# Kernel optimization log

Hardware: AMD Instinct MI355X
Metric: run time of the kernel (lower is better)

Reference implementation:

```python
import jax, jax.numpy as jnp
import numpy as np
from jax import lax

IN_F = 512   # encoder output dim
MEL = 80     # mel bins (memory_dim)
R = 7        # reduction factor
ATT = 128    # attention dim
B = 64
T_ENC = 512
T_MEL = 700  # must be divisible by R -> 100 decoder steps


def _gru(x, h, w_ih, w_hh, b_ih, b_hh):
    # torch.nn.GRUCell math
    gi = x @ w_ih.T + b_ih
    gh = h @ w_hh.T + b_hh
    ir, iz, inn = jnp.split(gi, 3, axis=-1)
    hr, hz, hn = jnp.split(gh, 3, axis=-1)
    r = jax.nn.sigmoid(ir + hr)
    z = jax.nn.sigmoid(iz + hz)
    return (1.0 - z) * jnp.tanh(inn + r * hn) + z * h


_PARAM_SHAPES = {
    'prenet_w1': (256, MEL), 'prenet_b1': (256,),
    'prenet_w2': (128, 256), 'prenet_b2': (128,),
    'attrnn_w_ih': (768, IN_F + 128), 'attrnn_w_hh': (768, 256),
    'attrnn_b_ih': (768,), 'attrnn_b_hh': (768,),
    'q_w': (ATT, 256), 'inp_w': (ATT, IN_F), 'v_w': (1, ATT), 'v_b': (1,),
    'loc_conv': (32, 2, 31), 'loc_w': (ATT, 32),
    'pd_w': (256, 256 + IN_F), 'pd_b': (256,),
    'dec1_w_ih': (768, 256), 'dec1_w_hh': (768, 256), 'dec1_b_ih': (768,), 'dec1_b_hh': (768,),
    'dec2_w_ih': (768, 256), 'dec2_w_hh': (768, 256), 'dec2_b_ih': (768,), 'dec2_b_hh': (768,),
    'mel_w': (MEL * R, 256), 'mel_b': (MEL * R,),
    'stop_w': (1, 256 + MEL * R), 'stop_b': (1,),
}


def setup_inputs() -> dict:
    key = jax.random.key(0)
    ks = iter(jax.random.split(key, 40))
    d = {
        'inputs': jax.random.normal(next(ks), (B, T_ENC, IN_F), jnp.float32),
        'memory': jax.random.normal(next(ks), (B, T_MEL, MEL), jnp.float32),
        'mask': jnp.ones((B, T_ENC), dtype=bool),
    }
    for n, s in _PARAM_SHAPES.items():
        d[n] = jax.random.normal(next(ks), s, jnp.float32) * 0.02
    return d


def reference(inputs, memory, mask, prenet_w1, prenet_b1, prenet_w2, prenet_b2,
              attrnn_w_ih, attrnn_w_hh, attrnn_b_ih, attrnn_b_hh,
              q_w, inp_w, v_w, v_b, loc_conv, loc_w, pd_w, pd_b,
              dec1_w_ih, dec1_w_hh, dec1_b_ih, dec1_b_hh,
              dec2_w_ih, dec2_w_hh, dec2_b_ih, dec2_b_hh,
              mel_w, mel_b, stop_w, stop_b):
    Bq, T_enc, _ = inputs.shape
    # attention.preprocess_inputs: [B, T_enc, ATT], computed once
    proc_in = jnp.einsum('btd,ad->bta', inputs, inp_w)
    # _reshape_memory: [B, T_mel, MEL] -> [T_steps, B, R*MEL]
    mem = memory.reshape(Bq, -1, R * MEL).transpose(1, 0, 2)
    # teacher forcing: step 0 uses zero memory_input, step t uses frame t-1
    xs = jnp.concatenate([jnp.zeros_like(mem[:1]), mem[:-1]], axis=0)

    def step(carry, x):
        h_att, h1, h2, ctx, aw, awc = carry
        # memory_size<=0 path: keep last mel frame of previous group
        m_in = x[:, MEL * (R - 1):]
        # prenet (original, dropout disabled)
        p = jax.nn.relu(m_in @ prenet_w1.T + prenet_b1)
        p = jax.nn.relu(p @ prenet_w2.T + prenet_b2)
        # attention RNN
        h_att = _gru(jnp.concatenate([p, ctx], axis=-1), h_att,
                     attrnn_w_ih, attrnn_w_hh, attrnn_b_ih, attrnn_b_hh)
        # location-sensitive attention
        pq = h_att @ q_w.T                              # [B, ATT]
        loc = jnp.stack([aw, awc], axis=1)              # [B, 2, T_enc]
        pl = lax.conv_general_dilated(loc, loc_conv, (1,), [(15, 15)],
                                      dimension_numbers=('NCH', 'OIH', 'NCH'))
        pl = jnp.einsum('bct,ac->bta', pl, loc_w)       # [B, T_enc, ATT]
        e = (jnp.tanh(pq[:, None, :] + proc_in + pl) @ v_w.T)[..., 0] + v_b
        e = jnp.where(mask, e, -1e9)
        align = jax.nn.softmax(e, axis=-1)              # [B, T_enc]
        ctx = jnp.einsum('bt,btd->bd', align, inputs)   # [B, IN_F]
        awc = awc + align
        # decoder RNNs with residual connections
        dec = jnp.concatenate([h_att, ctx], axis=-1) @ pd_w.T + pd_b
        h1 = _gru(dec, h1, dec1_w_ih, dec1_w_hh, dec1_b_ih, dec1_b_hh)
        dec = h1 + dec
        h2 = _gru(dec, h2, dec2_w_ih, dec2_w_hh, dec2_b_ih, dec2_b_hh)
        dec = h2 + dec
        out = dec @ mel_w.T + mel_b                     # [B, R*MEL]
        # separate_stopnet=True: stopnet input is detached
        sin = lax.stop_gradient(jnp.concatenate([dec, out], axis=-1))
        stop = (sin @ stop_w.T + stop_b)[:, 0]
        return (h_att, h1, h2, ctx, align, awc), (out, align, stop)

    z = lambda n: jnp.zeros((Bq, n), inputs.dtype)
    zt = jnp.zeros((Bq, T_enc), inputs.dtype)
    carry0 = (z(256), z(256), z(256), z(IN_F), zt, zt)
    _, (outs, atts, stops) = lax.scan(step, carry0, xs)
    # _parse_outputs
    outputs = outs.transpose(1, 0, 2).reshape(Bq, -1, MEL).transpose(0, 2, 1)  # [B, MEL, T_mel]
    return outputs, atts.transpose(1, 0, 2), stops.T
```

## Files before the change

### kernel.cpp

```cpp
#include <hip/hip_runtime.h>
#include <hip/hip_bf16.h>


typedef unsigned int u32;

#ifndef __has_builtin
#define __has_builtin(x) 0
#endif

#define NSTEP 100

#define PK_ATTIH 0
#define PK_ATTHH 245760
#define PK_Q     344064
#define PK_PD    360448
#define PK_D1IH  458752
#define PK_D1HH  557056
#define PK_D2IH  655360
#define PK_D2HH  753664
#define PK_MEL   851968
#define W1T_U    923648
#define W2T_U    944128
#define PROCF_U  976896
#define P2ALL_U  3074048

#define OUT_ATT  3584000
#define OUT_STOP 6860800

typedef _Float16 h2 __attribute__((ext_vector_type(2)));
union U4 { uint4 v; _Float16 h[8]; };

__device__ __forceinline__ float fastrcp(float x) { return __builtin_amdgcn_rcpf(x); }
__device__ __forceinline__ float sig_p(float x) { return 1.f / (1.f + __expf(-x)); }
__device__ __forceinline__ float tanh_f(float x) {
    x = fminf(fmaxf(x, -15.f), 15.f);
    float e2 = __expf(2.f * x);
    return (e2 - 1.f) * fastrcp(e2 + 1.f);
}

__device__ __forceinline__ float dot2(u32 w, u32 x, float acc) {
    h2 wh = __builtin_bit_cast(h2, w);
    h2 xh = __builtin_bit_cast(h2, x);
#if __has_builtin(__builtin_amdgcn_fdot2)
    return __builtin_amdgcn_fdot2(wh, xh, acc, false);
#else
    return acc + (float)wh.x * (float)xh.x + (float)wh.y * (float)xh.y;
#endif
}

__device__ __forceinline__ u32 packh2(float a, float b) {
    h2 h; h.x = (_Float16)a; h.y = (_Float16)b;
    return __builtin_bit_cast(u32, h);
}

__global__ void tkern(const float* __restrict__ src, float* __restrict__ dst, int O, int K) {
    int i = blockIdx.x * blockDim.x + threadIdx.x;
    if (i < O * K) {
        int o = i % O, k = i / O;
        dst[i] = src[o * K + k];
    }
}

__global__ void packw(const float* __restrict__ src, u32* __restrict__ dst, int O, int K) {
    int i = blockIdx.x * blockDim.x + threadIdx.x;
    int n = O * (K >> 1);
    if (i < n) {
        int o = i % O, p = i / O;
        dst[i] = packh2(src[o * K + 2 * p], src[o * K + 2 * p + 1]);
    }
}

__global__ void prenet_kern(const float* __restrict__ memory,
                            const float* __restrict__ w1T, const float* __restrict__ b1,
                            const float* __restrict__ w2T, const float* __restrict__ b2,
                            float* __restrict__ p2all) {
    __shared__ float mi[80];
    __shared__ float p1[256];
    int blk = blockIdx.x;
    int t = blk >> 6, b = blk & 63;
    int tid = threadIdx.x;
    if (tid < 80) mi[tid] = (t == 0) ? 0.f : memory[(b * 700 + (7 * t - 1)) * 80 + tid];
    __syncthreads();
    float acc = b1[tid];
#pragma unroll 4
    for (int k = 0; k < 80; k++) acc += mi[k] * w1T[k * 256 + tid];
    p1[tid] = fmaxf(acc, 0.f);
    __syncthreads();
    if (tid < 128) {
        float a2 = b2[tid];
#pragma unroll 4
        for (int k = 0; k < 256; k++) a2 += p1[k] * w2T[k * 128 + tid];
        p2all[(t * 64 + b) * 128 + tid] = fmaxf(a2, 0.f);
    }
}

__global__ void proc_kern(const float* __restrict__ inputs, const float* __restrict__ inpT,
                          _Float16* __restrict__ procF) {
    __shared__ float xin[8][512];
    int blk = blockIdx.x;
    int b = blk >> 6, t0 = (blk & 63) << 3;
    int tid = threadIdx.x;
    for (int i = tid; i < 8 * 512; i += 1024)
        xin[i >> 9][i & 511] = inputs[((size_t)b * 512 + t0 + (i >> 9)) * 512 + (i & 511)];
    __syncthreads();
    int r = tid >> 7, a = tid & 127;
    float acc = 0.f;
#pragma unroll 4
    for (int d = 0; d < 512; d++) acc += xin[r][d] * inpT[d * 128 + a];
    procF[((size_t)(b * 512) + t0 + r) * 128 + a] = (_Float16)acc;
}

__launch_bounds__(1024, 1)
__global__ void decoder_kern(const float* __restrict__ inputs,
                             const u32* __restrict__ wsu,
                             const float* __restrict__ att_b_ih, const float* __restrict__ att_b_hh,
                             const float* __restrict__ v_w, const float* __restrict__ v_b,
                             const float* __restrict__ lcg, const float* __restrict__ lwg,
                             const float* __restrict__ pd_b,
                             const float* __restrict__ d1b_ih, const float* __restrict__ d1b_hh,
                             const float* __restrict__ d2b_ih, const float* __restrict__ d2b_hh,
                             const float* __restrict__ mel_b,
                             const float* __restrict__ stop_w, const float* __restrict__ stop_b,
                             float* __restrict__ out) {
    const int b = blockIdx.x;
    const int tid = threadIdx.x;

    const uint4* w_attih = (const uint4*)(wsu + PK_ATTIH);
    const uint4* w_atthh = (const uint4*)(wsu + PK_ATTHH);
    const uint4* w_q     = (const uint4*)(wsu + PK_Q);
    const uint4* w_pd    = (const uint4*)(wsu + PK_PD);
    const uint4* w_d1ih  = (const uint4*)(wsu + PK_D1IH);
    const uint4* w_d1hh  = (const uint4*)(wsu + PK_D1HH);
    const uint4* w_d2ih  = (const uint4*)(wsu + PK_D2IH);
    const uint4* w_d2hh  = (const uint4*)(wsu + PK_D2HH);
    const uint4* w_mel   = (const uint4*)(wsu + PK_MEL);
    const _Float16* procF = (const _Float16*)(wsu + PROCF_U);
    const float* p2all   = (const float*)(wsu + P2ALL_U);

    __shared__ float h_att[256], h1[256], h2[256], dec[256];
    __shared__ float awp[542], awcp[542];
    __shared__ float pq[128], ebuf[512], red[32], mout[560];
    __shared__ float convbuf[32 * 513];
    __shared__ __align__(16) float scrA[4096];
    __shared__ __align__(16) float scrB[3072];
    __shared__ u32 xpatt[320];
    __shared__ u32 xppd[384];
    __shared__ u32 decp[128], h1p[128], h2p[128];

    for (int i = tid; i < 256; i += 1024) { h_att[i] = 0.f; h1[i] = 0.f; h2[i] = 0.f; dec[i] = 0.f; }
    for (int i = tid; i < 542; i += 1024) { awp[i] = 0.f; awcp[i] = 0.f; }
    for (int i = tid; i < 320; i += 1024) xpatt[i] = 0u;
    for (int i = tid; i < 384; i += 1024) xppd[i] = 0u;
    if (tid < 128) { decp[tid] = 0u; h1p[tid] = 0u; h2p[tid] = 0u; }
    if (tid >= 960) {
        int j = tid - 960;
        xpatt[j] = packh2(p2all[(size_t)b * 128 + 2 * j], p2all[(size_t)b * 128 + 2 * j + 1]);
    }
    const float vb0 = v_b[0];
    const float sb0 = stop_b[0];
    __syncthreads();

    for (int step = 0; step < NSTEP; step++) {
        if (tid < 768) {
            const int og = tid % 192;
            const int ks = tid / 192;
            float4 ai = {0.f, 0.f, 0.f, 0.f};
            float4 ah4 = {0.f, 0.f, 0.f, 0.f};
#pragma unroll 8
            for (int p = ks * 80; p < ks * 80 + 80; p++) {
                uint4 w = w_attih[p * 192 + og];
                u32 x = xpatt[p];
                ai.x = dot2(w.x, x, ai.x); ai.y = dot2(w.y, x, ai.y);
                ai.z = dot2(w.z, x, ai.z); ai.w = dot2(w.w, x, ai.w);
            }
#pragma unroll 8
            for (int p = ks * 32; p < ks * 32 + 32; p++) {
                uint4 w = w_atthh[p * 192 + og];
                u32 x = xppd[p];
                ah4.x = dot2(w.x, x, ah4.x); ah4.y = dot2(w.y, x, ah4.y);
                ah4.z = dot2(w.z, x, ah4.z); ah4.w = dot2(w.w, x, ah4.w);
            }
            *(float4*)&scrA[ks * 768 + og * 4] = ai;
            *(float4*)&scrB[ks * 768 + og * 4] = ah4;
        }
        __syncthreads();

        if (tid < 128) {
            float hv[2];
#pragma unroll
            for (int j = 0; j < 2; j++) {
                const int o = tid * 2 + j;
                float gr = att_b_ih[o], gz = att_b_ih[256 + o], gn = att_b_ih[512 + o];
                float hr = att_b_hh[o], hz = att_b_hh[256 + o], hn = att_b_hh[512 + o];
#pragma unroll
                for (int s = 0; s < 4; s++) {
                    gr += scrA[s * 768 + o]; gz += scrA[s * 768 + 256 + o]; gn += scrA[s * 768 + 512 + o];
                    hr += scrB[s * 768 + o]; hz += scrB[s * 768 + 256 + o]; hn += scrB[s * 768 + 512 + o];
                }
                float r = sig_p(gr + hr), z = sig_p(gz + hz);
                float n = tanhf(gn + r * hn);
                hv[j] = (1.f - z) * n + z * h_att[o];
                h_att[o] = hv[j];
            }
            xppd[tid] = packh2(hv[0], hv[1]);
        }
        __syncthreads();

        if (tid < 128) {
            const int og = tid & 31, ks = tid >> 5;
            float4 acc = {0.f, 0.f, 0.f, 0.f};
#pragma unroll 8
            for (int p = ks * 32; p < ks * 32 + 32; p++) {
                uint4 w = w_q[p * 32 + og];
                u32 x = xppd[p];
                acc.x = dot2(w.x, x, acc.x); acc.y = dot2(w.y, x, acc.y);
                acc.z = dot2(w.z, x, acc.z); acc.w = dot2(w.w, x, acc.w);
            }
            *(float4*)&scrA[ks * 128 + og * 4] = acc;
        } else if (tid >= 512) {
            const int tp = tid - 512;
            float cr[32];
#pragma unroll
            for (int c = 0; c < 32; c++) cr[c] = 0.f;
            for (int k = 0; k < 31; k++) {
                float a1 = awp[tp + k], a2 = awcp[tp + k];
#pragma unroll
                for (int c = 0; c < 32; c++)
                    cr[c] += lcg[c * 62 + k] * a1 + lcg[c * 62 + 31 + k] * a2;
            }
#pragma unroll
            for (int c = 0; c < 32; c++) convbuf[c * 513 + tp] = cr[c];
        }
        __syncthreads();

        if (tid < 128) {
            pq[tid] = scrA[tid] + scrA[128 + tid] + scrA[256 + tid] + scrA[384 + tid];
        }
        __syncthreads();

        {
            const int tp = tid & 511;
            const int ah = tid >> 9;
            const int a0 = ah * 64;
            float cr2[32];
#pragma unroll
            for (int c = 0; c < 32; c++) cr2[c] = convbuf[c * 513 + tp];
            const uint4* pf4 = (const uint4*)(procF + ((size_t)(b * 512 + tp)) * 128 + a0);
            float acc = 0.f;
            for (int l = 0; l < 8; l++) {
                U4 u; u.v = pf4[l];
#pragma unroll
                for (int j = 0; j < 8; j++) {
                    const int a = l * 8 + j;
                    float s = pq[a0 + a] + (float)u.h[j];
#pragma unroll
                    for (int c = 0; c < 32; c++) s += lwg[(a0 + a) * 32 + c] * cr2[c];
                    acc += v_w[a0 + a] * tanh_f(s);
                }
            }
            scrB[tid] = acc;
        }
        __syncthreads();

        float e_reg = -1e30f;
        if (tid < 512) e_reg = scrB[tid] + scrB[512 + tid] + vb0;
        {
            float v = e_reg;
#pragma unroll
            for (int off = 32; off; off >>= 1) v = fmaxf(v, __shfl_down(v, off, 64));
            if (tid < 512 && (tid & 63) == 0) red[tid >> 6] = v;
        }
        __syncthreads();
        if (tid == 0) {
            float m = red[0];
            for (int w = 1; w < 8; w++) m = fmaxf(m, red[w]);
            red[16] = m;
        }
        __syncthreads();
        float ex = 0.f;
        if (tid < 512) ex = __expf(e_reg - red[16]);
        {
            float v = ex;
#pragma unroll
            for (int off = 32; off; off >>= 1) v += __shfl_down(v, off, 64);
            if (tid < 512 && (tid & 63) == 0) red[tid >> 6] = v;
        }
        __syncthreads();
        if (tid == 0) {
            float s = 0.f;
            for (int w = 0; w < 8; w++) s += red[w];
            red[17] = s;
        }
        __syncthreads();
        if (tid < 512) {
            float al = ex * fastrcp(red[17]);
            ebuf[tid] = al;
            awp[15 + tid] = al;
            awcp[15 + tid] += al;
            out[OUT_ATT + ((size_t)b * 100 + step) * 512 + tid] = al;
        }
        __syncthreads();

        {
            const int dg = tid & 127, ts = tid >> 7;
            const float4* ib = (const float4*)(inputs + ((size_t)b * 512 + ts * 64) * 512);
            float4 acc = {0.f, 0.f, 0.f, 0.f};
#pragma unroll 8
            for (int t = 0; t < 64; t++) {
                float al = ebuf[ts * 64 + t];
                float4 xv = ib[(size_t)t * 128 + dg];
                acc.x += al * xv.x; acc.y += al * xv.y; acc.z += al * xv.z; acc.w += al * xv.w;
            }
            *(float4*)&scrA[ts * 512 + dg * 4] = acc;
        }
        __syncthreads();

        if (tid < 256) {
            float s0 = 0.f, s1 = 0.f;
#pragma unroll
            for (int q = 0; q < 8; q++) { s0 += scrA[q * 512 + 2 * tid]; s1 += scrA[q * 512 + 2 * tid + 1]; }
            u32 pr = packh2(s0, s1);
            xpatt[64 + tid] = pr;
            xppd[128 + tid] = pr;
        }
        __syncthreads();

        {
            const int og = tid & 63, ks = tid >> 6;
            float4 acc = {0.f, 0.f, 0.f, 0.f};
#pragma unroll 8
            for (int p = ks * 24; p < ks * 24 + 24; p++) {
                uint4 w = w_pd[p * 64 + og];
                u32 x = xppd[p];
                acc.x = dot2(w.x, x, acc.x); acc.y = dot2(w.y, x, acc.y);
                acc.z = dot2(w.z, x, acc.z); acc.w = dot2(w.w, x, acc.w);
            }
            *(float4*)&scrA[ks * 256 + og * 4] = acc;
        }
        __syncthreads();

        if (tid < 128) {
            float d0 = pd_b[2 * tid], d1 = pd_b[2 * tid + 1];
#pragma unroll
            for (int q = 0; q < 16; q++) { d0 += scrA[q * 256 + 2 * tid]; d1 += scrA[q * 256 + 2 * tid + 1]; }
            dec[2 * tid] = d0; dec[2 * tid + 1] = d1;
            decp[tid] = packh2(d0, d1);
        }
        __syncthreads();

        if (tid < 768) {
            const int og = tid % 192;
            const int ks = tid / 192;
            float4 ai = {0.f, 0.f, 0.f, 0.f};
            float4 ah4 = {0.f, 0.f, 0.f, 0.f};
#pragma unroll 8
            for (int p = ks * 32; p < ks * 32 + 32; p++) {
                uint4 w1 = w_d1ih[p * 192 + og];
                uint4 w2 = w_d1hh[p * 192 + og];
                u32 xd = decp[p], xh = h1p[p];
                ai.x = dot2(w1.x, xd, ai.x); ai.y = dot2(w1.y, xd, ai.y);
                ai.z = dot2(w1.z, xd, ai.z); ai.w = dot2(w1.w, xd, ai.w);
                ah4.x = dot2(w2.x, xh, ah4.x); ah4.y = dot2(w2.y, xh, ah4.y);
                ah4.z = dot2(w2.z, xh, ah4.z); ah4.w = dot2(w2.w, xh, ah4.w);
            }
            *(float4*)&scrA[ks * 768 + og * 4] = ai;
            *(float4*)&scrB[ks * 768 + og * 4] = ah4;
        }
        __syncthreads();

        if (tid < 128) {
            float hv[2], dv[2];
#pragma unroll
            for (int j = 0; j < 2; j++) {
                const int o = tid * 2 + j;
                float gr = d1b_ih[o], gz = d1b_ih[256 + o], gn = d1b_ih[512 + o];
                float hr = d1b_hh[o], hz = d1b_hh[256 + o], hn = d1b_hh[512 + o];
#pragma unroll
                for (int s = 0; s < 4; s++) {
                    gr += scrA[s * 768 + o]; gz += scrA[s * 768 + 256 + o]; gn += scrA[s * 768 + 512 + o];
                    hr += scrB[s * 768 + o]; hz += scrB[s * 768 + 256 + o]; hn += scrB[s * 768 + 512 + o];
                }
                float r = sig_p(gr + hr), z = sig_p(gz + hz);
                float n = tanhf(gn + r * hn);
                hv[j] = (1.f - z) * n + z * h1[o];
                h1[o] = hv[j];
                dv[j] = hv[j] + dec[o];
                dec[o] = dv[j];
            }
            h1p[tid] = packh2(hv[0], hv[1]);
            decp[tid] = packh2(dv[0], dv[1]);
        }
        __syncthreads();

        if (tid < 768) {
            const int og = tid % 192;
            const int ks = tid / 192;
            float4 ai = {0.f, 0.f, 0.f, 0.f};
            float4 ah4 = {0.f, 0.f, 0.f, 0.f};
#pragma unroll 8
            for (int p = ks * 32; p < ks * 32 + 32; p++) {
                uint4 w1 = w_d2ih[p * 192 + og];
                uint4 w2 = w_d2hh[p * 192 + og];
                u32 xd = decp[p], xh = h2p[p];
                ai.x = dot2(w1.x, xd, ai.x); ai.y = dot2(w1.y, xd, ai.y);
                ai.z = dot2(w1.z, xd, ai.z); ai.w = dot2(w1.w, xd, ai.w);
                ah4.x = dot2(w2.x, xh, ah4.x); ah4.y = dot2(w2.y, xh, ah4.y);
                ah4.z = dot2(w2.z, xh, ah4.z); ah4.w = dot2(w2.w, xh, ah4.w);
            }
            *(float4*)&scrA[ks * 768 + og * 4] = ai;
            *(float4*)&scrB[ks * 768 + og * 4] = ah4;
        }
        __syncthreads();

        if (tid < 128) {
            float hv[2], dv[2];
#pragma unroll
            for (int j = 0; j < 2; j++) {
                const int o = tid * 2 + j;
                float gr = d2b_ih[o], gz = d2b_ih[256 + o], gn = d2b_ih[512 + o];
                float hr = d2b_hh[o], hz = d2b_hh[256 + o], hn = d2b_hh[512 + o];
#pragma unroll
                for (int s = 0; s < 4; s++) {
                    gr += scrA[s * 768 + o]; gz += scrA[s * 768 + 256 + o]; gn += scrA[s * 768 + 512 + o];
                    hr += scrB[s * 768 + o]; hz += scrB[s * 768 + 256 + o]; hn += scrB[s * 768 + 512 + o];
                }
                float r = sig_p(gr + hr), z = sig_p(gz + hz);
                float n = tanhf(gn + r * hn);
                hv[j] = (1.f - z) * n + z * h2[o];
                h2[o] = hv[j];
                dv[j] = hv[j] + dec[o];
                dec[o] = dv[j];
            }
            h2p[tid] = packh2(hv[0], hv[1]);
            decp[tid] = packh2(dv[0], dv[1]);
        }
        __syncthreads();

        if (tid < 560) {
            const int og = tid % 140;
            const int ks = tid / 140;
            float4 acc = {0.f, 0.f, 0.f, 0.f};
#pragma unroll 8
            for (int p = ks * 32; p < ks * 32 + 32; p++) {
                uint4 w = w_mel[p * 140 + og];
                u32 x = decp[p];
                acc.x = dot2(w.x, x, acc.x); acc.y = dot2(w.y, x, acc.y);
                acc.z = dot2(w.z, x, acc.z); acc.w = dot2(w.w, x, acc.w);
            }
            *(float4*)&scrA[ks * 560 + og * 4] = acc;
        }
        __syncthreads();

        if (tid < 280) {
#pragma unroll
            for (int j = 0; j < 2; j++) {
                const int o = 2 * tid + j;
                float m = mel_b[o];
#pragma unroll
                for (int s = 0; s < 4; s++) m += scrA[s * 560 + o];
                mout[o] = m;
                int mm = o % 80, jj = o / 80;
                out[((size_t)b * 80 + mm) * 700 + 7 * step + jj] = m;
            }
        }
        __syncthreads();

        {
            float v = 0.f;
            if (tid < 816) v = ((tid < 256) ? dec[tid] : mout[tid - 256]) * stop_w[tid];
            if (tid < 832) {
#pragma unroll
                for (int off = 32; off; off >>= 1) v += __shfl_down(v, off, 64);
                if ((tid & 63) == 0) red[tid >> 6] = v;
            }
            if (tid >= 960 && step + 1 < NSTEP) {
                int j = tid - 960;
                const float* p2n = p2all + ((size_t)(step + 1) * 64 + b) * 128;
                xpatt[j] = packh2(p2n[2 * j], p2n[2 * j + 1]);
            }
        }
        __syncthreads();
        if (tid == 0) {
            float s = sb0;
            for (int w = 0; w < 13; w++) s += red[w];
            out[OUT_STOP + (size_t)b * 100 + step] = s;
        }
        __syncthreads();
    }
}

extern "C" void kernel_launch(void* const* d_in, const int* in_sizes, int n_in,
                              void* d_out, int out_size, void* d_ws, size_t ws_size,
                              hipStream_t stream) {
    const float* inputs    = (const float*)d_in[0];
    const float* memory    = (const float*)d_in[1];
    const float* prenet_w1 = (const float*)d_in[3];
    const float* prenet_b1 = (const float*)d_in[4];
    const float* prenet_w2 = (const float*)d_in[5];
    const float* prenet_b2 = (const float*)d_in[6];
    const float* att_w_ih  = (const float*)d_in[7];
    const float* att_w_hh  = (const float*)d_in[8];
    const float* att_b_ih  = (const float*)d_in[9];
    const float* att_b_hh  = (const float*)d_in[10];
    const float* q_w       = (const float*)d_in[11];
    const float* inp_w     = (const float*)d_in[12];
    const float* v_w       = (const float*)d_in[13];
    const float* v_b       = (const float*)d_in[14];
    const float* loc_conv  = (const float*)d_in[15];
    const float* loc_w     = (const float*)d_in[16];
    const float* pd_w      = (const float*)d_in[17];
    const float* pd_b      = (const float*)d_in[18];
    const float* d1_w_ih   = (const float*)d_in[19];
    const float* d1_w_hh   = (const float*)d_in[20];
    const float* d1_b_ih   = (const float*)d_in[21];
    const float* d1_b_hh   = (const float*)d_in[22];
    const float* d2_w_ih   = (const float*)d_in[23];
    const float* d2_w_hh   = (const float*)d_in[24];
    const float* d2_b_ih   = (const float*)d_in[25];
    const float* d2_b_hh   = (const float*)d_in[26];
    const float* mel_w     = (const float*)d_in[27];
    const float* mel_b     = (const float*)d_in[28];
    const float* stop_w    = (const float*)d_in[29];
    const float* stop_b    = (const float*)d_in[30];

    u32* wsu = (u32*)d_ws;
    float* out = (float*)d_out;

    auto P = [&](const float* src, int off, int O, int K) {
        int n = O * (K / 2);
        packw<<<(n + 255) / 256, 256, 0, stream>>>(src, wsu + off, O, K);
    };
    P(att_w_ih, PK_ATTIH, 768, 640);
    P(att_w_hh, PK_ATTHH, 768, 256);
    P(q_w,      PK_Q,     128, 256);
    P(pd_w,     PK_PD,    256, 768);
    P(d1_w_ih,  PK_D1IH,  768, 256);
    P(d1_w_hh,  PK_D1HH,  768, 256);
    P(d2_w_ih,  PK_D2IH,  768, 256);
    P(d2_w_hh,  PK_D2HH,  768, 256);
    P(mel_w,    PK_MEL,   560, 256);

    tkern<<<(256 * 80 + 255) / 256, 256, 0, stream>>>(prenet_w1, (float*)(wsu + W1T_U), 256, 80);
    tkern<<<(128 * 256 + 255) / 256, 256, 0, stream>>>(prenet_w2, (float*)(wsu + W2T_U), 128, 256);

    prenet_kern<<<6400, 256, 0, stream>>>(memory, (float*)(wsu + W1T_U), prenet_b1,
                                          (float*)(wsu + W2T_U), prenet_b2,
                                          (float*)(wsu + P2ALL_U));

    {
        float* inpT = (float*)(wsu + P2ALL_U + 819200);
        tkern<<<(128 * 512 + 255) / 256, 256, 0, stream>>>(inp_w, inpT, 128, 512);
        proc_kern<<<4096, 1024, 0, stream>>>(inputs, inpT, (_Float16*)(wsu + PROCF_U));
    }

    decoder_kern<<<64, 1024, 0, stream>>>(inputs, wsu,
                                          att_b_ih, att_b_hh, v_w, v_b,
                                          loc_conv, loc_w, pd_b,
                                          d1_b_ih, d1_b_hh, d2_b_ih, d2_b_hh,
                                          mel_b, stop_w, stop_b, out);
}
```

Measured before the change: 17.63 ms.

## Split each batch decoder across four blocks with global grid barriers

The persistent decoder goes from one 1024-thread block per batch element to four 512-thread blocks per element, 256 in total. Each block owns a quarter of the GRU outputs and of the encoder timesteps for attention. Recurrent state moves to workspace global memory, and blocks synchronise through an atomic-counter grid barrier several times per step. GRU weights are repacked so r/z/n gates sit together per output, and the attention softmax is reduced across blocks. This spreads the serial decoder over more compute units, but adds global-memory round trips and barrier latency on every step, and the spin barrier relies on all 256 blocks being resident at once.

```diff
diff --git a/kernel.cpp b/kernel.cpp
--- a/kernel.cpp
+++ b/kernel.cpp
@@ -10,24 +10,47 @@
 
 #define NSTEP 100
 
-#define PK_ATTIH 0
-#define PK_ATTHH 245760
-#define PK_Q     344064
-#define PK_PD    360448
-#define PK_D1IH  458752
-#define PK_D1HH  557056
-#define PK_D2IH  655360
-#define PK_D2HH  753664
-#define PK_MEL   851968
-#define W1T_U    923648
-#define W2T_U    944128
-#define PROCF_U  976896
-#define P2ALL_U  3074048
+#define ATTIH4_U 0
+#define ATTHH4_U 327680
+#define D1IH4_U  458752
+#define D1HH4_U  589824
+#define D2IH4_U  720896
+#define D2HH4_U  851968
+#define PKQ_U    983040
+#define PKPD_U   999424
+#define PKMEL_U  1097728
+#define W1T_U    1169408
+#define W2T_U    1189888
+#define INPT_U   1222656
+#define PROCF_U  1288192
+#define P2ALL_U  3385344
+#define HATT_U   4204544
+#define H1_U     4220928
+#define H2_U     4237312
+#define HATTP_U  4253696
+#define H1P_U    4261888
+#define H2P_U    4270080
+#define DEC0_U   4278272
+#define DEC1_U   4294656
+#define DEC2_U   4311040
+#define DEC0P_U  4327424
+#define DEC1P_U  4335616
+#define DEC2P_U  4343808
+#define CTXP_U   4352000
+#define XCATP_U  4483072
+#define ALIGN_U  4503552
+#define AWC_U    4536320
+#define SRED_U   4569088
+#define SRED2_U  4569600
+#define CNT_U    4570112
+#define STATE_BASE_U 4204544
+#define STATE_N   365632
+#define XCATP_REL 278528
 
 #define OUT_ATT  3584000
 #define OUT_STOP 6860800
 
-typedef _Float16 h2 __attribute__((ext_vector_type(2)));
+typedef _Float16 fh2 __attribute__((ext_vector_type(2)));
 union U4 { uint4 v; _Float16 h[8]; };
 
 __device__ __forceinline__ float fastrcp(float x) { return __builtin_amdgcn_rcpf(x); }
@@ -37,28 +60,37 @@
     float e2 = __expf(2.f * x);
     return (e2 - 1.f) * fastrcp(e2 + 1.f);
 }
-
 __device__ __forceinline__ float dot2(u32 w, u32 x, float acc) {
-    h2 wh = __builtin_bit_cast(h2, w);
-    h2 xh = __builtin_bit_cast(h2, x);
+    fh2 wh = __builtin_bit_cast(fh2, w);
+    fh2 xh = __builtin_bit_cast(fh2, x);
 #if __has_builtin(__builtin_amdgcn_fdot2)
     return __builtin_amdgcn_fdot2(wh, xh, acc, false);
 #else
     return acc + (float)wh.x * (float)xh.x + (float)wh.y * (float)xh.y;
 #endif
 }
-
 __device__ __forceinline__ u32 packh2(float a, float b) {
-    h2 h; h.x = (_Float16)a; h.y = (_Float16)b;
+    fh2 h; h.x = (_Float16)a; h.y = (_Float16)b;
     return __builtin_bit_cast(u32, h);
 }
+
+__device__ __forceinline__ void gridbar(u32* cnt, u32 target, int tid) {
+    __syncthreads();
+    if (tid == 0) {
+        __threadfence();
+        __hip_atomic_fetch_add(cnt, 1u, __ATOMIC_ACQ_REL, __HIP_MEMORY_SCOPE_AGENT);
+        while (__hip_atomic_load(cnt, __ATOMIC_ACQUIRE, __HIP_MEMORY_SCOPE_AGENT) < target) {
+            __builtin_amdgcn_s_sleep(1);
+        }
+        __threadfence();
+    }
+    __syncthreads();
+}
+
 
 __global__ void tkern(const float* __restrict__ src, float* __restrict__ dst, int O, int K) {
     int i = blockIdx.x * blockDim.x + threadIdx.x;
-    if (i < O * K) {
-        int o = i % O, k = i / O;
-        dst[i] = src[o * K + k];
-    }
+    if (i < O * K) { int o = i % O, k = i / O; dst[i] = src[o * K + k]; }
 }
 
 __global__ void packw(const float* __restrict__ src, u32* __restrict__ dst, int O, int K) {
@@ -67,6 +99,19 @@
     if (i < n) {
         int o = i % O, p = i / O;
         dst[i] = packh2(src[o * K + 2 * p], src[o * K + 2 * p + 1]);
+    }
+}
+
+__global__ void packg(const float* __restrict__ src, u32* __restrict__ dst, int K) {
+    int i = blockIdx.x * blockDim.x + threadIdx.x;
+    int P = K >> 1;
+    if (i < P * 256) {
+        int o = i & 255, p = i >> 8;
+        u32* d = dst + (size_t)i * 4;
+#pragma unroll
+        for (int g = 0; g < 3; g++)
+            d[g] = packh2(src[(g * 256 + o) * K + 2 * p], src[(g * 256 + o) * K + 2 * p + 1]);
+        d[3] = 0u;
     }
 }
 
@@ -110,382 +155,427 @@
     procF[((size_t)(b * 512) + t0 + r) * 128 + a] = (_Float16)acc;
 }
 
-__launch_bounds__(1024, 1)
-__global__ void decoder_kern(const float* __restrict__ inputs,
-                             const u32* __restrict__ wsu,
-                             const float* __restrict__ att_b_ih, const float* __restrict__ att_b_hh,
-                             const float* __restrict__ v_w, const float* __restrict__ v_b,
-                             const float* __restrict__ lcg, const float* __restrict__ lwg,
-                             const float* __restrict__ pd_b,
-                             const float* __restrict__ d1b_ih, const float* __restrict__ d1b_hh,
-                             const float* __restrict__ d2b_ih, const float* __restrict__ d2b_hh,
-                             const float* __restrict__ mel_b,
-                             const float* __restrict__ stop_w, const float* __restrict__ stop_b,
-                             float* __restrict__ out) {
-    const int b = blockIdx.x;
+__global__ void init_kern(u32* __restrict__ ws) {
+    int i = blockIdx.x * blockDim.x + threadIdx.x;
+    if (i >= STATE_N) return;
+    u32 v = 0u;
+    int j = i - XCATP_REL;
+    if (j >= 0 && j < 20480) {
+        int b = j / 320, k = j % 320;
+        if (k < 64) {
+            const float* p2 = (const float*)(ws + P2ALL_U) + (size_t)b * 128;
+            v = packh2(p2[2 * k], p2[2 * k + 1]);
+        }
+    }
+    ws[STATE_BASE_U + i] = v;
+}
+
+
+__launch_bounds__(512, 4)
+__global__ void decoder2(const float* __restrict__ inputs,
+                         u32* __restrict__ ws,
+                         const float* __restrict__ att_b_ih, const float* __restrict__ att_b_hh,
+                         const float* __restrict__ v_w, const float* __restrict__ v_b,
+                         const float* __restrict__ lcg, const float* __restrict__ lwg,
+                         const float* __restrict__ pd_b,
+                         const float* __restrict__ d1b_ih, const float* __restrict__ d1b_hh,
+                         const float* __restrict__ d2b_ih, const float* __restrict__ d2b_hh,
+                         const float* __restrict__ mel_b,
+                         const float* __restrict__ stop_w, const float* __restrict__ stop_b,
+                         float* __restrict__ out) {
+    const int B = blockIdx.x;
     const int tid = threadIdx.x;
-
-    const uint4* w_attih = (const uint4*)(wsu + PK_ATTIH);
-    const uint4* w_atthh = (const uint4*)(wsu + PK_ATTHH);
-    const uint4* w_q     = (const uint4*)(wsu + PK_Q);
-    const uint4* w_pd    = (const uint4*)(wsu + PK_PD);
-    const uint4* w_d1ih  = (const uint4*)(wsu + PK_D1IH);
-    const uint4* w_d1hh  = (const uint4*)(wsu + PK_D1HH);
-    const uint4* w_d2ih  = (const uint4*)(wsu + PK_D2IH);
-    const uint4* w_d2hh  = (const uint4*)(wsu + PK_D2HH);
-    const uint4* w_mel   = (const uint4*)(wsu + PK_MEL);
-    const _Float16* procF = (const _Float16*)(wsu + PROCF_U);
-    const float* p2all   = (const float*)(wsu + P2ALL_U);
-
-    __shared__ float h_att[256], h1[256], h2[256], dec[256];
-    __shared__ float awp[542], awcp[542];
-    __shared__ float pq[128], ebuf[512], red[32], mout[560];
-    __shared__ float convbuf[32 * 513];
-    __shared__ __align__(16) float scrA[4096];
-    __shared__ __align__(16) float scrB[3072];
-    __shared__ u32 xpatt[320];
-    __shared__ u32 xppd[384];
-    __shared__ u32 decp[128], h1p[128], h2p[128];
-
-    for (int i = tid; i < 256; i += 1024) { h_att[i] = 0.f; h1[i] = 0.f; h2[i] = 0.f; dec[i] = 0.f; }
-    for (int i = tid; i < 542; i += 1024) { awp[i] = 0.f; awcp[i] = 0.f; }
-    for (int i = tid; i < 320; i += 1024) xpatt[i] = 0u;
-    for (int i = tid; i < 384; i += 1024) xppd[i] = 0u;
-    if (tid < 128) { decp[tid] = 0u; h1p[tid] = 0u; h2p[tid] = 0u; }
-    if (tid >= 960) {
-        int j = tid - 960;
-        xpatt[j] = packh2(p2all[(size_t)b * 128 + 2 * j], p2all[(size_t)b * 128 + 2 * j + 1]);
-    }
+    const int b  = B >> 2;
+    const int os = B & 3;
+    const int t0 = os * 128;
+    const int lane = tid & 63;
+    const int wv = tid >> 6;
+
+    const uint4* wA   = (const uint4*)(ws + ATTIH4_U);
+    const uint4* wAH  = (const uint4*)(ws + ATTHH4_U);
+    const uint4* w1I  = (const uint4*)(ws + D1IH4_U);
+    const uint4* w1H  = (const uint4*)(ws + D1HH4_U);
+    const uint4* w2I  = (const uint4*)(ws + D2IH4_U);
+    const uint4* w2H  = (const uint4*)(ws + D2HH4_U);
+    const u32* wQ     = ws + PKQ_U;
+    const u32* wPD    = ws + PKPD_U;
+    const u32* wMEL   = ws + PKMEL_U;
+    const _Float16* procF = (const _Float16*)(ws + PROCF_U);
+    const float* p2all = (const float*)(ws + P2ALL_U);
+    float* HATT = (float*)(ws + HATT_U);
+    float* H1   = (float*)(ws + H1_U);
+    float* H2   = (float*)(ws + H2_U);
+    u32* HATTP  = ws + HATTP_U;
+    u32* H1P    = ws + H1P_U;
+    u32* H2P    = ws + H2P_U;
+    float* DEC0 = (float*)(ws + DEC0_U);
+    float* DEC1 = (float*)(ws + DEC1_U);
+    float* DEC2 = (float*)(ws + DEC2_U);
+    u32* DEC0P  = ws + DEC0P_U;
+    u32* DEC1P  = ws + DEC1P_U;
+    u32* DEC2P  = ws + DEC2P_U;
+    float* CTXP = (float*)(ws + CTXP_U);
+    u32* XCATP  = ws + XCATP_U;
+    float* ALGN = (float*)(ws + ALIGN_U);
+    float* AWC  = (float*)(ws + AWC_U);
+    float* SRED = (float*)(ws + SRED_U);
+    float* SRED2= (float*)(ws + SRED2_U);
+    u32* cnt    = ws + CNT_U;
+
+    __shared__ float lc[1984];
+    __shared__ float eb[128];
+    __shared__ u32 xc[320];
+    __shared__ u32 xhp[128];
+    __shared__ float scr6[3072];
+    __shared__ float hb[64], db[64];
+    __shared__ float aw[158], awc[158];
+    __shared__ float convbuf[32 * 132];
+    __shared__ float pq[128];
+    __shared__ float scrE[512];
+    __shared__ float redv[8];
+    __shared__ float ms[2];
+    __shared__ float alb[128];
+    __shared__ float scrC[2048];
+    __shared__ u32 xp[384];
+    __shared__ u32 dp[128], hp[128];
+    __shared__ float scrG[420];
+    __shared__ float mo[140];
+
+    for (int i = tid; i < 1984; i += 512) lc[i] = lcg[i];
     const float vb0 = v_b[0];
     const float sb0 = stop_b[0];
+    u32 ph = 0;
     __syncthreads();
 
     for (int step = 0; step < NSTEP; step++) {
-        if (tid < 768) {
-            const int og = tid % 192;
-            const int ks = tid / 192;
-            float4 ai = {0.f, 0.f, 0.f, 0.f};
-            float4 ah4 = {0.f, 0.f, 0.f, 0.f};
-#pragma unroll 8
-            for (int p = ks * 80; p < ks * 80 + 80; p++) {
-                uint4 w = w_attih[p * 192 + og];
-                u32 x = xpatt[p];
-                ai.x = dot2(w.x, x, ai.x); ai.y = dot2(w.y, x, ai.y);
-                ai.z = dot2(w.z, x, ai.z); ai.w = dot2(w.w, x, ai.w);
-            }
-#pragma unroll 8
-            for (int p = ks * 32; p < ks * 32 + 32; p++) {
-                uint4 w = w_atthh[p * 192 + og];
-                u32 x = xppd[p];
-                ah4.x = dot2(w.x, x, ah4.x); ah4.y = dot2(w.y, x, ah4.y);
-                ah4.z = dot2(w.z, x, ah4.z); ah4.w = dot2(w.w, x, ah4.w);
-            }
-            *(float4*)&scrA[ks * 768 + og * 4] = ai;
-            *(float4*)&scrB[ks * 768 + og * 4] = ah4;
-        }
-        __syncthreads();
-
+        if (tid < 320) xc[tid] = XCATP[b * 320 + tid];
+        else if (tid < 448) xhp[tid - 320] = HATTP[b * 128 + (tid - 320)];
+        __syncthreads();
+        {
+            float air = 0.f, aiz = 0.f, ain = 0.f, ahr = 0.f, ahz = 0.f, ahn = 0.f;
+            const int oabs = os * 64 + lane;
+#pragma unroll 8
+            for (int p = wv * 40; p < wv * 40 + 40; p++) {
+                uint4 w = wA[p * 256 + oabs];
+                u32 x = xc[p];
+                air = dot2(w.x, x, air); aiz = dot2(w.y, x, aiz); ain = dot2(w.z, x, ain);
+            }
+#pragma unroll 8
+            for (int p = wv * 16; p < wv * 16 + 16; p++) {
+                uint4 w = wAH[p * 256 + oabs];
+                u32 x = xhp[p];
+                ahr = dot2(w.x, x, ahr); ahz = dot2(w.y, x, ahz); ahn = dot2(w.z, x, ahn);
+            }
+            float* s = &scr6[wv * 384 + lane];
+            s[0] = air; s[64] = aiz; s[128] = ain; s[192] = ahr; s[256] = ahz; s[320] = ahn;
+        }
+        __syncthreads();
+        if (tid < 64) {
+            const int oabs = os * 64 + tid;
+            float gr = att_b_ih[oabs], gz = att_b_ih[256 + oabs], gn = att_b_ih[512 + oabs];
+            float hr = att_b_hh[oabs], hz = att_b_hh[256 + oabs], hn = att_b_hh[512 + oabs];
+#pragma unroll
+            for (int k = 0; k < 8; k++) {
+                const float* s = &scr6[k * 384 + tid];
+                gr += s[0]; gz += s[64]; gn += s[128];
+                hr += s[192]; hz += s[256]; hn += s[320];
+            }
+            float r = sig_p(gr + hr), z = sig_p(gz + hz);
+            float n = tanhf(gn + r * hn);
+            float h = (1.f - z) * n + z * HATT[b * 256 + oabs];
+            HATT[b * 256 + oabs] = h;
+            hb[tid] = h;
+        }
+        __syncthreads();
+        if (tid < 32) HATTP[b * 128 + os * 32 + tid] = packh2(hb[2 * tid], hb[2 * tid + 1]);
+        ++ph; gridbar(cnt, 256u * ph, tid);
+
+        if (tid < 128) xhp[tid] = HATTP[b * 128 + tid];
+        else if (tid < 286) {
+            int j = tid - 128, t = t0 + j - 15;
+            aw[j] = (t >= 0 && t < 512) ? ALGN[b * 512 + t] : 0.f;
+        } else if (tid < 444) {
+            int j = tid - 286, t = t0 + j - 15;
+            awc[j] = (t >= 0 && t < 512) ? AWC[b * 512 + t] : 0.f;
+        }
+        __syncthreads();
+        {
+            const int n = tid & 127, ks = tid >> 7;
+            float acc = 0.f;
+#pragma unroll 8
+            for (int p = ks * 32; p < ks * 32 + 32; p++)
+                acc = dot2(wQ[p * 128 + n], xhp[p], acc);
+            scrE[ks * 128 + n] = acc;
+        }
+        __syncthreads();
+        {
+            const int tl = tid & 127, cs = tid >> 7;
+#pragma unroll
+            for (int c = cs * 8; c < cs * 8 + 8; c++) {
+                float s = 0.f;
+                const float* l1 = &lc[c * 62];
+#pragma unroll
+                for (int k = 0; k < 31; k++) s += l1[k] * aw[tl + k] + l1[31 + k] * awc[tl + k];
+                convbuf[c * 132 + tl] = s;
+            }
+            if (tid < 128) pq[tid] = scrE[tid] + scrE[128 + tid] + scrE[256 + tid] + scrE[384 + tid];
+        }
+        __syncthreads();
+        {
+            const int tl = tid & 127, as = tid >> 7;
+            const int a0 = as * 32;
+            float cr[32];
+#pragma unroll
+            for (int c = 0; c < 32; c++) cr[c] = convbuf[c * 132 + tl];
+            const uint4* pf = (const uint4*)(procF + ((size_t)(b * 512) + t0 + tl) * 128 + a0);
+            float acc = 0.f;
+#pragma unroll
+            for (int l = 0; l < 4; l++) {
+                U4 u; u.v = pf[l];
+#pragma unroll
+                for (int j = 0; j < 8; j++) {
+                    const int a = a0 + l * 8 + j;
+                    float s = pq[a] + (float)u.h[j];
+#pragma unroll
+                    for (int c = 0; c < 32; c++) s += lwg[a * 32 + c] * cr[c];
+                    acc += v_w[a] * tanh_f(s);
+                }
+            }
+            scrE[as * 128 + tl] = acc;
+        }
+        __syncthreads();
         if (tid < 128) {
-            float hv[2];
-#pragma unroll
-            for (int j = 0; j < 2; j++) {
-                const int o = tid * 2 + j;
-                float gr = att_b_ih[o], gz = att_b_ih[256 + o], gn = att_b_ih[512 + o];
-                float hr = att_b_hh[o], hz = att_b_hh[256 + o], hn = att_b_hh[512 + o];
-#pragma unroll
-                for (int s = 0; s < 4; s++) {
-                    gr += scrA[s * 768 + o]; gz += scrA[s * 768 + 256 + o]; gn += scrA[s * 768 + 512 + o];
-                    hr += scrB[s * 768 + o]; hz += scrB[s * 768 + 256 + o]; hn += scrB[s * 768 + 512 + o];
-                }
-                float r = sig_p(gr + hr), z = sig_p(gz + hz);
-                float n = tanhf(gn + r * hn);
-                hv[j] = (1.f - z) * n + z * h_att[o];
-                h_att[o] = hv[j];
-            }
-            xppd[tid] = packh2(hv[0], hv[1]);
-        }
-        __syncthreads();
-
+            float e = scrE[tid] + scrE[128 + tid] + scrE[256 + tid] + scrE[384 + tid] + vb0;
+            eb[tid] = e;
+            float v = e;
+#pragma unroll
+            for (int off = 32; off; off >>= 1) v = fmaxf(v, __shfl_down(v, off, 64));
+            if ((tid & 63) == 0) redv[tid >> 6] = v;
+        }
+        __syncthreads();
         if (tid < 128) {
-            const int og = tid & 31, ks = tid >> 5;
+            float m_s = fmaxf(redv[0], redv[1]);
+            if (tid == 0) ms[0] = m_s;
+            float v = __expf(eb[tid] - m_s);
+#pragma unroll
+            for (int off = 32; off; off >>= 1) v += __shfl_down(v, off, 64);
+            if ((tid & 63) == 0) redv[2 + (tid >> 6)] = v;
+        }
+        __syncthreads();
+        if (tid == 0) {
+            SRED[b * 8 + os * 2]     = ms[0];
+            SRED[b * 8 + os * 2 + 1] = redv[2] + redv[3];
+        }
+        ++ph; gridbar(cnt, 256u * ph, tid);
+
+        if (tid == 0) {
+            float M = SRED[b * 8], S;
+            for (int s = 1; s < 4; s++) M = fmaxf(M, SRED[b * 8 + 2 * s]);
+            S = 0.f;
+            for (int s = 0; s < 4; s++) S += SRED[b * 8 + 2 * s + 1] * __expf(SRED[b * 8 + 2 * s] - M);
+            ms[0] = M; ms[1] = fastrcp(S);
+        }
+        __syncthreads();
+        if (tid < 128) {
+            float al = __expf(eb[tid] - ms[0]) * ms[1];
+            const int t = t0 + tid;
+            ALGN[b * 512 + t] = al;
+            AWC[b * 512 + t] += al;
+            out[OUT_ATT + ((size_t)b * 100 + step) * 512 + t] = al;
+            alb[tid] = al;
+        }
+        __syncthreads();
+        {
+            const int dg = tid & 127, tsl = tid >> 7;
+            const float4* in4 = (const float4*)inputs + ((size_t)(b * 512) + t0 + tsl * 32) * 128 + dg;
             float4 acc = {0.f, 0.f, 0.f, 0.f};
 #pragma unroll 8
-            for (int p = ks * 32; p < ks * 32 + 32; p++) {
-                uint4 w = w_q[p * 32 + og];
-                u32 x = xppd[p];
-                acc.x = dot2(w.x, x, acc.x); acc.y = dot2(w.y, x, acc.y);
-                acc.z = dot2(w.z, x, acc.z); acc.w = dot2(w.w, x, acc.w);
-            }
-            *(float4*)&scrA[ks * 128 + og * 4] = acc;
-        } else if (tid >= 512) {
-            const int tp = tid - 512;
-            float cr[32];
-#pragma unroll
-            for (int c = 0; c < 32; c++) cr[c] = 0.f;
-            for (int k = 0; k < 31; k++) {
-                float a1 = awp[tp + k], a2 = awcp[tp + k];
-#pragma unroll
-                for (int c = 0; c < 32; c++)
-                    cr[c] += lcg[c * 62 + k] * a1 + lcg[c * 62 + 31 + k] * a2;
-            }
-#pragma unroll
-            for (int c = 0; c < 32; c++) convbuf[c * 513 + tp] = cr[c];
-        }
-        __syncthreads();
-
-        if (tid < 128) {
-            pq[tid] = scrA[tid] + scrA[128 + tid] + scrA[256 + tid] + scrA[384 + tid];
-        }
-        __syncthreads();
-
-        {
-            const int tp = tid & 511;
-            const int ah = tid >> 9;
-            const int a0 = ah * 64;
-            float cr2[32];
-#pragma unroll
-            for (int c = 0; c < 32; c++) cr2[c] = convbuf[c * 513 + tp];
-            const uint4* pf4 = (const uint4*)(procF + ((size_t)(b * 512 + tp)) * 128 + a0);
+            for (int i = 0; i < 32; i++) {
+                float al = alb[tsl * 32 + i];
+                float4 x = in4[(size_t)i * 128];
+                acc.x += al * x.x; acc.y += al * x.y; acc.z += al * x.z; acc.w += al * x.w;
+            }
+            *(float4*)&scrC[tsl * 512 + dg * 4] = acc;
+        }
+        __syncthreads();
+        {
+            float s = scrC[tid] + scrC[512 + tid] + scrC[1024 + tid] + scrC[1536 + tid];
+            CTXP[((size_t)os * 64 + b) * 512 + tid] = s;
+        }
+        ++ph; gridbar(cnt, 256u * ph, tid);
+
+        if (tid < 256) {
+            const int j = tid;
+            float s0 = 0.f, s1 = 0.f;
+#pragma unroll
+            for (int s = 0; s < 4; s++) {
+                const float* cp = &CTXP[((size_t)s * 64 + b) * 512];
+                s0 += cp[2 * j]; s1 += cp[2 * j + 1];
+            }
+            u32 pr = packh2(s0, s1);
+            xp[128 + j] = pr;
+            if (os == 0) XCATP[b * 320 + 64 + j] = pr;
+        } else if (tid < 384) {
+            xp[tid - 256] = HATTP[b * 128 + (tid - 256)];
+        } else if (tid < 448 && os == 1 && step + 1 < NSTEP) {
+            int j = tid - 384;
+            const float* p2n = p2all + ((size_t)(step + 1) * 64 + b) * 128;
+            XCATP[b * 320 + j] = packh2(p2n[2 * j], p2n[2 * j + 1]);
+        }
+        __syncthreads();
+        {
+            const int oabs = os * 64 + lane;
             float acc = 0.f;
-            for (int l = 0; l < 8; l++) {
-                U4 u; u.v = pf4[l];
-#pragma unroll
-                for (int j = 0; j < 8; j++) {
-                    const int a = l * 8 + j;
-                    float s = pq[a0 + a] + (float)u.h[j];
-#pragma unroll
-                    for (int c = 0; c < 32; c++) s += lwg[(a0 + a) * 32 + c] * cr2[c];
-                    acc += v_w[a0 + a] * tanh_f(s);
-                }
-            }
-            scrB[tid] = acc;
-        }
-        __syncthreads();
-
-        float e_reg = -1e30f;
-        if (tid < 512) e_reg = scrB[tid] + scrB[512 + tid] + vb0;
-        {
-            float v = e_reg;
-#pragma unroll
-            for (int off = 32; off; off >>= 1) v = fmaxf(v, __shfl_down(v, off, 64));
-            if (tid < 512 && (tid & 63) == 0) red[tid >> 6] = v;
-        }
-        __syncthreads();
-        if (tid == 0) {
-            float m = red[0];
-            for (int w = 1; w < 8; w++) m = fmaxf(m, red[w]);
-            red[16] = m;
-        }
-        __syncthreads();
-        float ex = 0.f;
-        if (tid < 512) ex = __expf(e_reg - red[16]);
-        {
-            float v = ex;
+#pragma unroll 8
+            for (int p = wv * 48; p < wv * 48 + 48; p++)
+                acc = dot2(wPD[p * 256 + oabs], xp[p], acc);
+            scr6[wv * 64 + lane] = acc;
+        }
+        __syncthreads();
+        if (tid < 64) {
+            const int oabs = os * 64 + tid;
+            float d = pd_b[oabs];
+#pragma unroll
+            for (int k = 0; k < 8; k++) d += scr6[k * 64 + tid];
+            DEC0[b * 256 + oabs] = d;
+            db[tid] = d;
+        }
+        __syncthreads();
+        if (tid < 32) DEC0P[b * 128 + os * 32 + tid] = packh2(db[2 * tid], db[2 * tid + 1]);
+        ++ph; gridbar(cnt, 256u * ph, tid);
+
+        if (tid < 128) dp[tid] = DEC0P[b * 128 + tid];
+        else if (tid < 256) hp[tid - 128] = H1P[b * 128 + (tid - 128)];
+        __syncthreads();
+        {
+            float air = 0.f, aiz = 0.f, ain = 0.f, ahr = 0.f, ahz = 0.f, ahn = 0.f;
+            const int oabs = os * 64 + lane;
+#pragma unroll 8
+            for (int p = wv * 16; p < wv * 16 + 16; p++) {
+                uint4 wi = w1I[p * 256 + oabs];
+                uint4 wh = w1H[p * 256 + oabs];
+                u32 xd = dp[p], xh = hp[p];
+                air = dot2(wi.x, xd, air); aiz = dot2(wi.y, xd, aiz); ain = dot2(wi.z, xd, ain);
+                ahr = dot2(wh.x, xh, ahr); ahz = dot2(wh.y, xh, ahz); ahn = dot2(wh.z, xh, ahn);
+            }
+            float* s = &scr6[wv * 384 + lane];
+            s[0] = air; s[64] = aiz; s[128] = ain; s[192] = ahr; s[256] = ahz; s[320] = ahn;
+        }
+        __syncthreads();
+        if (tid < 64) {
+            const int oabs = os * 64 + tid;
+            float gr = d1b_ih[oabs], gz = d1b_ih[256 + oabs], gn = d1b_ih[512 + oabs];
+            float hr = d1b_hh[oabs], hz = d1b_hh[256 + oabs], hn = d1b_hh[512 + oabs];
+#pragma unroll
+            for (int k = 0; k < 8; k++) {
+                const float* s = &scr6[k * 384 + tid];
+                gr += s[0]; gz += s[64]; gn += s[128];
+                hr += s[192]; hz += s[256]; hn += s[320];
+            }
+            float r = sig_p(gr + hr), z = sig_p(gz + hz);
+            float n = tanhf(gn + r * hn);
+            float h = (1.f - z) * n + z * H1[b * 256 + oabs];
+            H1[b * 256 + oabs] = h;
+            float d = DEC0[b * 256 + oabs] + h;
+            DEC1[b * 256 + oabs] = d;
+            hb[tid] = h; db[tid] = d;
+        }
+        __syncthreads();
+        if (tid < 32) {
+            H1P[b * 128 + os * 32 + tid]   = packh2(hb[2 * tid], hb[2 * tid + 1]);
+            DEC1P[b * 128 + os * 32 + tid] = packh2(db[2 * tid], db[2 * tid + 1]);
+        }
+        ++ph; gridbar(cnt, 256u * ph, tid);
+
+        if (tid < 128) dp[tid] = DEC1P[b * 128 + tid];
+        else if (tid < 256) hp[tid - 128] = H2P[b * 128 + (tid - 128)];
+        __syncthreads();
+        {
+            float air = 0.f, aiz = 0.f, ain = 0.f, ahr = 0.f, ahz = 0.f, ahn = 0.f;
+            const int oabs = os * 64 + lane;
+#pragma unroll 8
+            for (int p = wv * 16; p < wv * 16 + 16; p++) {
+                uint4 wi = w2I[p * 256 + oabs];
+                uint4 wh = w2H[p * 256 + oabs];
+                u32 xd = dp[p], xh = hp[p];
+                air = dot2(wi.x, xd, air); aiz = dot2(wi.y, xd, aiz); ain = dot2(wi.z, xd, ain);
+                ahr = dot2(wh.x, xh, ahr); ahz = dot2(wh.y, xh, ahz); ahn = dot2(wh.z, xh, ahn);
+            }
+            float* s = &scr6[wv * 384 + lane];
+            s[0] = air; s[64] = aiz; s[128] = ain; s[192] = ahr; s[256] = ahz; s[320] = ahn;
+        }
+        __syncthreads();
+        if (tid < 64) {
+            const int oabs = os * 64 + tid;
+            float gr = d2b_ih[oabs], gz = d2b_ih[256 + oabs], gn = d2b_ih[512 + oabs];
+            float hr = d2b_hh[oabs], hz = d2b_hh[256 + oabs], hn = d2b_hh[512 + oabs];
+#pragma unroll
+            for (int k = 0; k < 8; k++) {
+                const float* s = &scr6[k * 384 + tid];
+                gr += s[0]; gz += s[64]; gn += s[128];
+                hr += s[192]; hz += s[256]; hn += s[320];
+            }
+            float r = sig_p(gr + hr), z = sig_p(gz + hz);
+            float n = tanhf(gn + r * hn);
+            float h = (1.f - z) * n + z * H2[b * 256 + oabs];
+            H2[b * 256 + oabs] = h;
+            float d = DEC1[b * 256 + oabs] + h;
+            DEC2[b * 256 + oabs] = d;
+            hb[tid] = h; db[tid] = d;
+        }
+        __syncthreads();
+        if (tid < 32) {
+            H2P[b * 128 + os * 32 + tid]   = packh2(hb[2 * tid], hb[2 * tid + 1]);
+            DEC2P[b * 128 + os * 32 + tid] = packh2(db[2 * tid], db[2 * tid + 1]);
+        }
+        ++ph; gridbar(cnt, 256u * ph, tid);
+
+        if (tid < 128) dp[tid] = DEC2P[b * 128 + tid];
+        __syncthreads();
+        if (tid < 420) {
+            const int oi = tid % 140, ks = tid / 140;
+            const int oabs = os * 140 + oi;
+            const int p0 = ks * 43, pc = (ks == 2) ? 42 : 43;
+            float acc = 0.f;
+#pragma unroll 8
+            for (int p = p0; p < p0 + pc; p++)
+                acc = dot2(wMEL[p * 560 + oabs], dp[p], acc);
+            scrG[ks * 140 + oi] = acc;
+        }
+        __syncthreads();
+        if (tid < 140) {
+            const int oabs = os * 140 + tid;
+            float m = mel_b[oabs] + scrG[tid] + scrG[140 + tid] + scrG[280 + tid];
+            mo[tid] = m;
+            int mm = oabs % 80, jj = oabs / 80;
+            out[((size_t)b * 80 + mm) * 700 + 7 * step + jj] = m;
+        }
+        __syncthreads();
+        if (tid < 64) {
+            const int l = tid;
+            float v = mo[l] * stop_w[256 + os * 140 + l]
+                    + mo[64 + l] * stop_w[256 + os * 140 + 64 + l];
+            if (l < 12) v += mo[128 + l] * stop_w[256 + os * 140 + 128 + l];
 #pragma unroll
             for (int off = 32; off; off >>= 1) v += __shfl_down(v, off, 64);
-            if (tid < 512 && (tid & 63) == 0) red[tid >> 6] = v;
-        }
-        __syncthreads();
-        if (tid == 0) {
-            float s = 0.f;
-            for (int w = 0; w < 8; w++) s += red[w];
-            red[17] = s;
-        }
-        __syncthreads();
-        if (tid < 512) {
-            float al = ex * fastrcp(red[17]);
-            ebuf[tid] = al;
-            awp[15 + tid] = al;
-            awcp[15 + tid] += al;
-            out[OUT_ATT + ((size_t)b * 100 + step) * 512 + tid] = al;
-        }
-        __syncthreads();
-
-        {
-            const int dg = tid & 127, ts = tid >> 7;
-            const float4* ib = (const float4*)(inputs + ((size_t)b * 512 + ts * 64) * 512);
-            float4 acc = {0.f, 0.f, 0.f, 0.f};
-#pragma unroll 8
-            for (int t = 0; t < 64; t++) {
-                float al = ebuf[ts * 64 + t];
-                float4 xv = ib[(size_t)t * 128 + dg];
-                acc.x += al * xv.x; acc.y += al * xv.y; acc.z += al * xv.z; acc.w += al * xv.w;
-            }
-            *(float4*)&scrA[ts * 512 + dg * 4] = acc;
-        }
-        __syncthreads();
-
-        if (tid < 256) {
-            float s0 = 0.f, s1 = 0.f;
-#pragma unroll
-            for (int q = 0; q < 8; q++) { s0 += scrA[q * 512 + 2 * tid]; s1 += scrA[q * 512 + 2 * tid + 1]; }
-            u32 pr = packh2(s0, s1);
-            xpatt[64 + tid] = pr;
-            xppd[128 + tid] = pr;
-        }
-        __syncthreads();
-
-        {
-            const int og = tid & 63, ks = tid >> 6;
-            float4 acc = {0.f, 0.f, 0.f, 0.f};
-#pragma unroll 8
-            for (int p = ks * 24; p < ks * 24 + 24; p++) {
-                uint4 w = w_pd[p * 64 + og];
-                u32 x = xppd[p];
-                acc.x = dot2(w.x, x, acc.x); acc.y = dot2(w.y, x, acc.y);
-                acc.z = dot2(w.z, x, acc.z); acc.w = dot2(w.w, x, acc.w);
-            }
-            *(float4*)&scrA[ks * 256 + og * 4] = acc;
-        }
-        __syncthreads();
-
-        if (tid < 128) {
-            float d0 = pd_b[2 * tid], d1 = pd_b[2 * tid + 1];
-#pragma unroll
-            for (int q = 0; q < 16; q++) { d0 += scrA[q * 256 + 2 * tid]; d1 += scrA[q * 256 + 2 * tid + 1]; }
-            dec[2 * tid] = d0; dec[2 * tid + 1] = d1;
-            decp[tid] = packh2(d0, d1);
-        }
-        __syncthreads();
-
-        if (tid < 768) {
-            const int og = tid % 192;
-            const int ks = tid / 192;
-            float4 ai = {0.f, 0.f, 0.f, 0.f};
-            float4 ah4 = {0.f, 0.f, 0.f, 0.f};
-#pragma unroll 8
-            for (int p = ks * 32; p < ks * 32 + 32; p++) {
-                uint4 w1 = w_d1ih[p * 192 + og];
-                uint4 w2 = w_d1hh[p * 192 + og];
-                u32 xd = decp[p], xh = h1p[p];
-                ai.x = dot2(w1.x, xd, ai.x); ai.y = dot2(w1.y, xd, ai.y);
-                ai.z = dot2(w1.z, xd, ai.z); ai.w = dot2(w1.w, xd, ai.w);
-                ah4.x = dot2(w2.x, xh, ah4.x); ah4.y = dot2(w2.y, xh, ah4.y);
-                ah4.z = dot2(w2.z, xh, ah4.z); ah4.w = dot2(w2.w, xh, ah4.w);
-            }
-            *(float4*)&scrA[ks * 768 + og * 4] = ai;
-            *(float4*)&scrB[ks * 768 + og * 4] = ah4;
-        }
-        __syncthreads();
-
-        if (tid < 128) {
-            float hv[2], dv[2];
-#pragma unroll
-            for (int j = 0; j < 2; j++) {
-                const int o = tid * 2 + j;
-                float gr = d1b_ih[o], gz = d1b_ih[256 + o], gn = d1b_ih[512 + o];
-                float hr = d1b_hh[o], hz = d1b_hh[256 + o], hn = d1b_hh[512 + o];
-#pragma unroll
-                for (int s = 0; s < 4; s++) {
-                    gr += scrA[s * 768 + o]; gz += scrA[s * 768 + 256 + o]; gn += scrA[s * 768 + 512 + o];
-                    hr += scrB[s * 768 + o]; hz += scrB[s * 768 + 256 + o]; hn += scrB[s * 768 + 512 + o];
-                }
-                float r = sig_p(gr + hr), z = sig_p(gz + hz);
-                float n = tanhf(gn + r * hn);
-                hv[j] = (1.f - z) * n + z * h1[o];
-                h1[o] = hv[j];
-                dv[j] = hv[j] + dec[o];
-                dec[o] = dv[j];
-            }
-            h1p[tid] = packh2(hv[0], hv[1]);
-            decp[tid] = packh2(dv[0], dv[1]);
-        }
-        __syncthreads();
-
-        if (tid < 768) {
-            const int og = tid % 192;
-            const int ks = tid / 192;
-            float4 ai = {0.f, 0.f, 0.f, 0.f};
-            float4 ah4 = {0.f, 0.f, 0.f, 0.f};
-#pragma unroll 8
-            for (int p = ks * 32; p < ks * 32 + 32; p++) {
-                uint4 w1 = w_d2ih[p * 192 + og];
-                uint4 w2 = w_d2hh[p * 192 + og];
-                u32 xd = decp[p], xh = h2p[p];
-                ai.x = dot2(w1.x, xd, ai.x); ai.y = dot2(w1.y, xd, ai.y);
-                ai.z = dot2(w1.z, xd, ai.z); ai.w = dot2(w1.w, xd, ai.w);
-                ah4.x = dot2(w2.x, xh, ah4.x); ah4.y = dot2(w2.y, xh, ah4.y);
-                ah4.z = dot2(w2.z, xh, ah4.z); ah4.w = dot2(w2.w, xh, ah4.w);
-            }
-            *(float4*)&scrA[ks * 768 + og * 4] = ai;
-            *(float4*)&scrB[ks * 768 + og * 4] = ah4;
-        }
-        __syncthreads();
-
-        if (tid < 128) {
-            float hv[2], dv[2];
-#pragma unroll
-            for (int j = 0; j < 2; j++) {
-                const int o = tid * 2 + j;
-                float gr = d2b_ih[o], gz = d2b_ih[256 + o], gn = d2b_ih[512 + o];
-                float hr = d2b_hh[o], hz = d2b_hh[256 + o], hn = d2b_hh[512 + o];
-#pragma unroll
-                for (int s = 0; s < 4; s++) {
-                    gr += scrA[s * 768 + o]; gz += scrA[s * 768 + 256 + o]; gn += scrA[s * 768 + 512 + o];
-                    hr += scrB[s * 768 + o]; hz += scrB[s * 768 + 256 + o]; hn += scrB[s * 768 + 512 + o];
-                }
-                float r = sig_p(gr + hr), z = sig_p(gz + hz);
-                float n = tanhf(gn + r * hn);
-                hv[j] = (1.f - z) * n + z * h2[o];
-                h2[o] = hv[j];
-                dv[j] = hv[j] + dec[o];
-                dec[o] = dv[j];
-            }
-            h2p[tid] = packh2(hv[0], hv[1]);
-            decp[tid] = packh2(dv[0], dv[1]);
-        }
-        __syncthreads();
-
-        if (tid < 560) {
-            const int og = tid % 140;
-            const int ks = tid / 140;
-            float4 acc = {0.f, 0.f, 0.f, 0.f};
-#pragma unroll 8
-            for (int p = ks * 32; p < ks * 32 + 32; p++) {
-                uint4 w = w_mel[p * 140 + og];
-                u32 x = decp[p];
-                acc.x = dot2(w.x, x, acc.x); acc.y = dot2(w.y, x, acc.y);
-                acc.z = dot2(w.z, x, acc.z); acc.w = dot2(w.w, x, acc.w);
-            }
-            *(float4*)&scrA[ks * 560 + og * 4] = acc;
-        }
-        __syncthreads();
-
-        if (tid < 280) {
-#pragma unroll
-            for (int j = 0; j < 2; j++) {
-                const int o = 2 * tid + j;
-                float m = mel_b[o];
-#pragma unroll
-                for (int s = 0; s < 4; s++) m += scrA[s * 560 + o];
-                mout[o] = m;
-                int mm = o % 80, jj = o / 80;
-                out[((size_t)b * 80 + mm) * 700 + 7 * step + jj] = m;
-            }
-        }
-        __syncthreads();
-
-        {
+            if (l == 0) SRED2[b * 8 + os] = v;
+        } else if (tid < 128 && os == 0) {
+            const int l = tid - 64;
             float v = 0.f;
-            if (tid < 816) v = ((tid < 256) ? dec[tid] : mout[tid - 256]) * stop_w[tid];
-            if (tid < 832) {
-#pragma unroll
-                for (int off = 32; off; off >>= 1) v += __shfl_down(v, off, 64);
-                if ((tid & 63) == 0) red[tid >> 6] = v;
-            }
-            if (tid >= 960 && step + 1 < NSTEP) {
-                int j = tid - 960;
-                const float* p2n = p2all + ((size_t)(step + 1) * 64 + b) * 128;
-                xpatt[j] = packh2(p2n[2 * j], p2n[2 * j + 1]);
-            }
-        }
-        __syncthreads();
-        if (tid == 0) {
-            float s = sb0;
-            for (int w = 0; w < 13; w++) s += red[w];
+#pragma unroll
+            for (int g = 0; g < 4; g++)
+                v += DEC2[b * 256 + l + 64 * g] * stop_w[l + 64 * g];
+#pragma unroll
+            for (int off = 32; off; off >>= 1) v += __shfl_down(v, off, 64);
+            if (l == 0) SRED2[b * 8 + 4] = v;
+        }
+        ++ph; gridbar(cnt, 256u * ph, tid);
+
+        if (os == 0 && tid == 0) {
+            float s = sb0 + SRED2[b * 8] + SRED2[b * 8 + 1] + SRED2[b * 8 + 2]
+                    + SRED2[b * 8 + 3] + SRED2[b * 8 + 4];
             out[OUT_STOP + (size_t)b * 100 + step] = s;
         }
-        __syncthreads();
     }
 }
 
@@ -526,36 +616,29 @@
     u32* wsu = (u32*)d_ws;
     float* out = (float*)d_out;
 
-    auto P = [&](const float* src, int off, int O, int K) {
-        int n = O * (K / 2);
-        packw<<<(n + 255) / 256, 256, 0, stream>>>(src, wsu + off, O, K);
-    };
-    P(att_w_ih, PK_ATTIH, 768, 640);
-    P(att_w_hh, PK_ATTHH, 768, 256);
-    P(q_w,      PK_Q,     128, 256);
-    P(pd_w,     PK_PD,    256, 768);
-    P(d1_w_ih,  PK_D1IH,  768, 256);
-    P(d1_w_hh,  PK_D1HH,  768, 256);
-    P(d2_w_ih,  PK_D2IH,  768, 256);
-    P(d2_w_hh,  PK_D2HH,  768, 256);
-    P(mel_w,    PK_MEL,   560, 256);
-
+    packg<<<(320 * 256 + 255) / 256, 256, 0, stream>>>(att_w_ih, wsu + ATTIH4_U, 640);
+    packg<<<(128 * 256 + 255) / 256, 256, 0, stream>>>(att_w_hh, wsu + ATTHH4_U, 256);
+    packg<<<(128 * 256 + 255) / 256, 256, 0, stream>>>(d1_w_ih,  wsu + D1IH4_U, 256);
+    packg<<<(128 * 256 + 255) / 256, 256, 0, stream>>>(d1_w_hh,  wsu + D1HH4_U, 256);
+    packg<<<(128 * 256 + 255) / 256, 256, 0, stream>>>(d2_w_ih,  wsu + D2IH4_U, 256);
+    packg<<<(128 * 256 + 255) / 256, 256, 0, stream>>>(d2_w_hh,  wsu + D2HH4_U, 256);
+    packw<<<(128 * 128 + 255) / 256, 256, 0, stream>>>(q_w,   wsu + PKQ_U,   128, 256);
+    packw<<<(384 * 256 + 255) / 256, 256, 0, stream>>>(pd_w,  wsu + PKPD_U,  256, 768);
+    packw<<<(128 * 560 + 255) / 256, 256, 0, stream>>>(mel_w, wsu + PKMEL_U, 560, 256);
     tkern<<<(256 * 80 + 255) / 256, 256, 0, stream>>>(prenet_w1, (float*)(wsu + W1T_U), 256, 80);
     tkern<<<(128 * 256 + 255) / 256, 256, 0, stream>>>(prenet_w2, (float*)(wsu + W2T_U), 128, 256);
+    tkern<<<(128 * 512 + 255) / 256, 256, 0, stream>>>(inp_w, (float*)(wsu + INPT_U), 128, 512);
 
     prenet_kern<<<6400, 256, 0, stream>>>(memory, (float*)(wsu + W1T_U), prenet_b1,
                                           (float*)(wsu + W2T_U), prenet_b2,
                                           (float*)(wsu + P2ALL_U));
-
-    {
-        float* inpT = (float*)(wsu + P2ALL_U + 819200);
-        tkern<<<(128 * 512 + 255) / 256, 256, 0, stream>>>(inp_w, inpT, 128, 512);
-        proc_kern<<<4096, 1024, 0, stream>>>(inputs, inpT, (_Float16*)(wsu + PROCF_U));
-    }
-
-    decoder_kern<<<64, 1024, 0, stream>>>(inputs, wsu,
-                                          att_b_ih, att_b_hh, v_w, v_b,
-                                          loc_conv, loc_w, pd_b,
-                                          d1_b_ih, d1_b_hh, d2_b_ih, d2_b_hh,
-                                          mel_b, stop_w, stop_b, out);
-}
+    proc_kern<<<4096, 1024, 0, stream>>>(inputs, (float*)(wsu + INPT_U),
+                                         (_Float16*)(wsu + PROCF_U));
+    init_kern<<<(STATE_N + 255) / 256, 256, 0, stream>>>(wsu);
+
+    decoder2<<<256, 512, 0, stream>>>(inputs, wsu,
+                                      att_b_ih, att_b_hh, v_w, v_b,
+                                      loc_conv, loc_w, pd_b,
+                                      d1_b_ih, d1_b_hh, d2_b_ih, d2_b_hh,
+                                      mel_b, stop_w, stop_b, out);
+}
```

New measurement: 49.34 ms. +179.8%, slower.
